# Kernel optimization log

Measured on AMD Instinct MI355X. Metric: run time of the kernel, lower is better.

## Reference

```python
import jax, jax.numpy as jnp
import numpy as np
from jax import lax

# 19 edges over 19 body-joint heatmap channels (0..18); PAF channels are 19..56
EDGES = np.array([[1,8],[8,9],[9,10],[1,11],[11,12],[12,13],[1,2],[2,3],[3,4],[2,16],
                  [1,5],[5,6],[6,7],[5,17],[0,1],[0,14],[0,15],[14,16],[15,17]], dtype=np.int32)
_i = np.arange(19, dtype=np.int32)
# per-edge 4 input channels: [node_a, node_b, paf_x(=19+2i), paf_y(=20+2i)]
CH_IDX = np.concatenate([EDGES, (19 + 2*_i)[:, None], (20 + 2*_i)[:, None]], axis=1)  # [19,4]

_W_SHAPES = [(16,4,5,5),(16,16,5,5),(32,16,5,5),(32,32,5,5),(32,32,5,5),(128,32,1,1),(2,128,1,1)]

def _conv(x, w, b):
    p = (w.shape[-1] - 1) // 2  # padding=2 for 5x5, 0 for 1x1
    y = lax.conv_general_dilated(x, w, window_strides=(1,1), padding=[(p,p),(p,p)],
                                 dimension_numbers=('NCHW','OIHW','NCHW'))
    return y + b[None, :, None, None]

def setup_inputs() -> dict:
    key = jax.random.key(0)
    keys = jax.random.split(key, 1 + 2*len(_W_SHAPES))
    N, C, H, W = 16, 57, 128, 128
    inp = {'cnn_output': jax.random.normal(keys[0], (N, C, H, W), dtype=jnp.float32),
           'gnn_interations': 1}
    for i, s in enumerate(_W_SHAPES):
        inp[f'w{i}'] = jax.random.normal(keys[1+2*i], s, dtype=jnp.float32) * 0.01
        inp[f'b{i}'] = jax.random.normal(keys[2+2*i], (s[0],), dtype=jnp.float32) * 0.01
    return inp

def reference(cnn_output, gnn_interations, w0, b0, w1, b1, w2, b2, w3, b3, w4, b4, w5, b5, w6, b6):
    N, _, H, Wd = cnn_output.shape
    ws = (w0, w1, w2, w3, w4, w5, w6)
    bs = (b0, b1, b2, b3, b4, b5, b6)
    # gather per-edge 4-channel inputs: [N,19,4,H,W] -> fold edges into batch
    x = cnn_output[:, jnp.asarray(CH_IDX)]            # [N,19,4,H,W]
    x = x.reshape(N * 19, 4, H, Wd)
    for i in range(7):
        x = _conv(x, ws[i], bs[i])
        if i != 6:
            x = jax.nn.relu(x)
    # edge n output (2 ch) -> output channels [2n, 2n+1]
    return x.reshape(N, 38, H, Wd)
```

## Files before the change

### kernel.cpp

```cpp
#include <hip/hip_runtime.h>
#include <hip/hip_bf16.h>

typedef __bf16  bf16x8 __attribute__((ext_vector_type(8)));
typedef float   f32x4  __attribute__((ext_vector_type(4)));
typedef int     i32x4  __attribute__((ext_vector_type(4)));
typedef int     i32x8  __attribute__((ext_vector_type(8)));

__device__ __constant__ int EDGE_A[19] = {1,8,9,1,11,12,1,2,3,2,1,5,6,5,0,0,0,14,15};
__device__ __constant__ int EDGE_B[19] = {8,9,10,11,12,13,2,3,4,16,5,6,7,17,1,14,15,16,17};

#define SACT  64.0f
#define SINV  (1.0f / 4096.0f)
#define SREQ  0.015625f
#define SCL1  0x7F7F7F7F

__device__ __forceinline__ unsigned short f2bf(float f) {
    unsigned int x = __float_as_uint(f);
    x += 0x7FFFu + ((x >> 16) & 1u);
    return (unsigned short)(x >> 16);
}
__device__ __forceinline__ unsigned int pack2(float a, float b) {
    __hip_bfloat162 t = __float22bfloat162_rn(make_float2(a, b));
    unsigned int r; __builtin_memcpy(&r, &t, 4); return r;
}
__device__ __forceinline__ unsigned char f2fp8(float v) {
    int r = __builtin_amdgcn_cvt_pk_fp8_f32(v, 0.f, 0, false);
    return (unsigned char)(r & 0xff);
}
__device__ __forceinline__ unsigned int pk4fp8(float a, float b, float c, float d) {
    int v = __builtin_amdgcn_cvt_pk_fp8_f32(a, b, 0, false);
    v = __builtin_amdgcn_cvt_pk_fp8_f32(c, d, v, true);
    return (unsigned int)v;
}
__device__ __forceinline__ unsigned int quant4(f32x4 a, float4 b, float s, bool oob) {
    float v0 = fmaxf(fmaf(a[0], s, b.x), 0.f);
    float v1 = fmaxf(fmaf(a[1], s, b.y), 0.f);
    float v2 = fmaxf(fmaf(a[2], s, b.z), 0.f);
    float v3 = fmaxf(fmaf(a[3], s, b.w), 0.f);
    unsigned int v = pk4fp8(v0, v1, v2, v3);
    return oob ? 0u : v;
}

__device__ __forceinline__ int sw8 (int l) { return l ^ ((l >> 4) & 8);  }
__device__ __forceinline__ int sw48(int l) { return l ^ ((l >> 3) & 48); }

__device__ __forceinline__ void store_relu4(unsigned char* dst, f32x4 a, float4 b, bool oob) {
    unsigned int lo = pack2(fmaxf(a[0] + b.x, 0.f), fmaxf(a[1] + b.y, 0.f));
    unsigned int hi = pack2(fmaxf(a[2] + b.z, 0.f), fmaxf(a[3] + b.w, 0.f));
    uint2 v; v.x = oob ? 0u : lo; v.y = oob ? 0u : hi;
    *(uint2*)dst = v;
}

extern "C" __global__ void __launch_bounds__(256)
reorder_weights(const float* __restrict__ w0, const float* __restrict__ w1,
                const float* __restrict__ w2, const float* __restrict__ w3,
                const float* __restrict__ w4, const float* __restrict__ w5,
                unsigned char* __restrict__ ws)
{
    int idx = blockIdx.x * 256 + threadIdx.x;
    unsigned short* wsS = (unsigned short*)ws;
    if (idx < 4096) {
        int k = idx & 31, oc = idx >> 5;
        wsS[idx] = f2bf(w5[oc * 32 + k]);
    } else if (idx < 6144) {
        int j = idx - 4096;
        int k = j & 31, n = (j >> 5) & 15, c = j >> 9;
        int t = c * 8 + (k >> 2), ic = k & 3;
        float v = (t < 25) ? w0[(n * 4 + ic) * 25 + t] : 0.f;
        wsS[idx] = f2bf(v);
    }
    if (idx < 6656) {
        int k = idx & 31, n = (idx >> 5) & 15, tp = idx >> 9;
        int t = 2 * tp + (k >> 4), ic = k & 15;
        float v = (t < 25) ? w1[(n * 16 + ic) * 25 + t] * SACT : 0.f;
        ws[12288 + idx] = f2fp8(v);
    } else if (idx < 19968) {
        int j = idx - 6656;
        int k = j & 31, n = (j >> 5) & 15, nt = (j >> 9) & 1, tp = j >> 10;
        int t = 2 * tp + (k >> 4), ic = k & 15, oc = nt * 16 + n;
        float v = (t < 25) ? w2[(oc * 16 + ic) * 25 + t] * SACT : 0.f;
        ws[18944 + j] = f2fp8(v);
    } else if (idx < 48640) {
        int j = idx - 19968;
        int tg = j >> 12, r = j & 4095;
        int nt = r >> 11, n = (r >> 7) & 15, q = (r >> 5) & 3, ic = r & 31;
        int tap = 4 * tg + q;
        float v = (tap < 25) ? w3[((nt * 16 + n) * 32 + ic) * 25 + tap] * SACT : 0.f;
        ws[32256 + j] = f2fp8(v);
    } else if (idx < 77312) {
        int j = idx - 48640;
        int tg = j >> 12, r = j & 4095;
        int nt = r >> 11, n = (r >> 7) & 15, q = (r >> 5) & 3, ic = r & 31;
        int tap = 4 * tg + q;
        float v = (tap < 25) ? w4[((nt * 16 + n) * 32 + ic) * 25 + tap] * SACT : 0.f;
        ws[60928 + j] = f2fp8(v);
    }
}

__device__ __forceinline__ void conv0_slab(
    const unsigned short* __restrict__ s_in, unsigned char* __restrict__ s0,
    const unsigned char* __restrict__ wB, const float* __restrict__ b0,
    int yoff, int oy, int ox, int wave, int lane)
{
    const int nl = lane & 15, quad = lane >> 4;
    const unsigned short* w0p = (const unsigned short*)(wB + 8192);
    bf16x8 wf[4];
#pragma unroll
    for (int c = 0; c < 4; ++c)
        wf[c] = *(const bf16x8*)(w0p + c * 512 + nl * 32 + quad * 8);
    float4 bb = *(const float4*)(b0 + quad * 4);
    float4 bbs = make_float4(bb.x * SACT, bb.y * SACT, bb.z * SACT, bb.w * SACT);

    int coff0[4], coff1[4];
#pragma unroll
    for (int c = 0; c < 4; ++c) {
        int t0 = c * 8 + quad * 2, t1 = t0 + 1;
        if (t0 > 24) t0 = 24;
        if (t1 > 24) t1 = 24;
        coff0[c] = ((t0 / 5) * 36 + (t0 % 5)) * 8;
        coff1[c] = ((t1 / 5) * 36 + (t1 % 5)) * 8;
    }
    const unsigned char* sB = (const unsigned char*)s_in;

#pragma unroll 1
    for (int i = 0; i < 9; ++i) {
        int mt = wave + 4 * i;
        int p = mt * 16 + nl;
        int y = p >> 5, x = p & 31;
        int abase = (y * 36 + x) * 8;
        f32x4 acc = (f32x4)0.f;
#pragma unroll
        for (int c = 0; c < 4; ++c) {
            uint2 lo = *(const uint2*)(sB + abase + coff0[c]);
            uint2 hi = *(const uint2*)(sB + abase + coff1[c]);
            bf16x8 a;
            ((uint2*)&a)[0] = lo; ((uint2*)&a)[1] = hi;
            acc = __builtin_amdgcn_mfma_f32_16x16x32_bf16(wf[c], a, acc, 0, 0, 0);
        }
        bool oob = ((unsigned)(oy - 8 + y + yoff) >= 128u) || ((unsigned)(ox - 8 + x) >= 128u);
        *(unsigned int*)(s0 + sw8(p * 16 + quad * 4)) = quant4(acc, bbs, SACT, oob);
    }
}

__device__ __forceinline__ void conv1_fp8(
    const unsigned char* __restrict__ s0, unsigned char* __restrict__ s1,
    const unsigned char* __restrict__ wB, const float* __restrict__ b1,
    int POFF, int gy0, int gx0, int wave, int lane)
{
    const int nl = lane & 15, quad = lane >> 4;
    const int h = quad >> 1, g8 = (quad & 1) * 8;

    int abase[7];
#pragma unroll
    for (int i = 0; i < 7; ++i) {
        int p = (wave + 4 * i) * 16 + nl;
        if (p > 391) p = 391;
        int y = p / 28, x = p - y * 28;
        abase[i] = (y * 32 + x) * 16 + g8;
    }
    f32x4 acc[7];
#pragma unroll
    for (int i = 0; i < 7; ++i) acc[i] = (f32x4)0.f;

    const unsigned char* wp = wB + 12288 + nl * 32 + quad * 8;

#pragma unroll 1
    for (int c0 = 0; c0 < 13; c0 += 5) {
        long wl[5];
#pragma unroll
        for (int tp = 0; tp < 5; ++tp)
            if (c0 + tp < 13) wl[tp] = *(const long*)(wp + (c0 + tp) * 512);
#pragma unroll
        for (int tp = 0; tp < 5; ++tp) {
            if (c0 + tp < 13) {
                int t = 2 * (c0 + tp) + h;
                if (t > 24) t = 24;
                int dy = t / 5, dx = t - 5 * dy;
                int toff = (dy * 32 + dx) * 16;
#pragma unroll
                for (int i = 0; i < 7; ++i)
                    if (wave + 4 * i < 25) {
                        long a = *(const long*)(s0 + sw8(abase[i] + toff));
                        acc[i] = __builtin_amdgcn_mfma_f32_16x16x32_fp8_fp8(wl[tp], a, acc[i], 0, 0, 0);
                    }
            }
        }
    }

    float4 bb = *(const float4*)(b1 + quad * 4);
    float4 bbs = make_float4(bb.x * SACT, bb.y * SACT, bb.z * SACT, bb.w * SACT);
#pragma unroll
    for (int i = 0; i < 7; ++i) {
        int p = (wave + 4 * i) * 16 + nl;
        if (p < 392) {
            int pg = p + POFF;
            int y = pg / 28, x = pg - y * 28;
            bool oob = ((unsigned)(gy0 + y) >= 128u) || ((unsigned)(gx0 + x) >= 128u);
            *(unsigned int*)(s1 + sw8(pg * 16 + quad * 4)) = quant4(acc[i], bbs, SREQ, oob);
        }
    }
}

template<int I0, int NI>
__device__ __forceinline__ void conv2_fp8(
    const unsigned char* __restrict__ s1, unsigned char* __restrict__ s2,
    const unsigned char* __restrict__ wA, const float* __restrict__ b2,
    int gy0, int gx0, int wave, int lane)
{
    const int nl = lane & 15, quad = lane >> 4;
    const int h = quad >> 1, g8 = (quad & 1) * 8;

    int abase[NI];
#pragma unroll
    for (int i = 0; i < NI; ++i) {
        int p = (wave + 4 * (I0 + i)) * 16 + nl;
        int y = p / 24, x = p - y * 24;
        abase[i] = (y * 28 + x) * 16 + g8;
    }
    f32x4 acc[NI][2];
#pragma unroll
    for (int i = 0; i < NI; ++i) { acc[i][0] = (f32x4)0.f; acc[i][1] = (f32x4)0.f; }

    const unsigned char* wp = wA + nl * 32 + quad * 8;

#pragma unroll 1
    for (int c0 = 0; c0 < 13; c0 += 3) {
        long wl[3][2];
#pragma unroll
        for (int tp = 0; tp < 3; ++tp)
            if (c0 + tp < 13) {
                wl[tp][0] = *(const long*)(wp + ((c0 + tp) * 2 + 0) * 512);
                wl[tp][1] = *(const long*)(wp + ((c0 + tp) * 2 + 1) * 512);
            }
#pragma unroll
        for (int tp = 0; tp < 3; ++tp) {
            if (c0 + tp < 13) {
                int t = 2 * (c0 + tp) + h;
                if (t > 24) t = 24;
                int dy = t / 5, dx = t - 5 * dy;
                int toff = (dy * 28 + dx) * 16;
#pragma unroll
                for (int i = 0; i < NI; ++i) {
                    long a = *(const long*)(s1 + sw8(abase[i] + toff));
                    acc[i][0] = __builtin_amdgcn_mfma_f32_16x16x32_fp8_fp8(wl[tp][0], a, acc[i][0], 0, 0, 0);
                    acc[i][1] = __builtin_amdgcn_mfma_f32_16x16x32_fp8_fp8(wl[tp][1], a, acc[i][1], 0, 0, 0);
                }
            }
        }
    }

#pragma unroll
    for (int i = 0; i < NI; ++i) {
        int p = (wave + 4 * (I0 + i)) * 16 + nl;
        int y = p / 24, x = p - y * 24;
        bool oob = ((unsigned)(gy0 + y) >= 128u) || ((unsigned)(gx0 + x) >= 128u);
#pragma unroll
        for (int nt = 0; nt < 2; ++nt) {
            float4 bb = *(const float4*)(b2 + nt * 16 + quad * 4);
            float4 bbs = make_float4(bb.x * SACT, bb.y * SACT, bb.z * SACT, bb.w * SACT);
            *(unsigned int*)(s2 + p * 48 + nt * 16 + quad * 4) =
                quant4(acc[i][nt], bbs, SREQ, oob);
        }
    }
}

template<int SINW, int SOUT, int MAXM, bool GUARD, bool FP8OUT>
__device__ __forceinline__ void conv_c32_mx(
    const unsigned char* __restrict__ sinB, unsigned char* __restrict__ soutB,
    const unsigned char* __restrict__ wA, const float* __restrict__ bias,
    int gy0, int gx0, int wave, int lane)
{
    constexpr int NM = (SOUT * SOUT) / 16;
    const int nl = lane & 15, quad = lane >> 4;

    int abase[MAXM];
#pragma unroll
    for (int i = 0; i < MAXM; ++i) {
        int p = (wave + 4 * i) * 16 + nl;
        if (GUARD && p > SOUT * SOUT - 1) p = SOUT * SOUT - 1;
        int y = p / SOUT, x = p - y * SOUT;
        abase[i] = (y * SINW + x) * 48;
    }
    f32x4 acc[MAXM][2];
#pragma unroll
    for (int i = 0; i < MAXM; ++i) { acc[i][0] = (f32x4)0.f; acc[i][1] = (f32x4)0.f; }

    const unsigned char* wp = wA + nl * 128 + quad * 32;

#pragma unroll 1
    for (int tg = 0; tg < 7; ++tg) {
        int t = 4 * tg + quad;
        if (t > 24) t = 24;
        int dy = t / 5, dx = t - 5 * dy;
        int to = (dy * SINW + dx) * 48;
        i32x8 wl0 = *(const i32x8*)(wp + tg * 4096);
        i32x8 wl1 = *(const i32x8*)(wp + tg * 4096 + 2048);
#pragma unroll
        for (int i = 0; i < MAXM; ++i)
            if (!GUARD || wave + 4 * i < NM) {
                i32x4 alo = *(const i32x4*)(sinB + abase[i] + to);
                i32x4 ahi = *(const i32x4*)(sinB + abase[i] + to + 16);
                i32x8 a;
                ((i32x4*)&a)[0] = alo; ((i32x4*)&a)[1] = ahi;
                acc[i][0] = __builtin_amdgcn_mfma_scale_f32_16x16x128_f8f6f4(
                                wl0, a, acc[i][0], 0, 0, 0, SCL1, 0, SCL1);
                acc[i][1] = __builtin_amdgcn_mfma_scale_f32_16x16x128_f8f6f4(
                                wl1, a, acc[i][1], 0, 0, 0, SCL1, 0, SCL1);
            }
    }

#pragma unroll
    for (int i = 0; i < MAXM; ++i) {
        int p = (wave + 4 * i) * 16 + nl;
        if (!GUARD || p < SOUT * SOUT) {
            int y = p / SOUT, x = p - y * SOUT;
            bool oob = ((unsigned)(gy0 + y) >= 128u) || ((unsigned)(gx0 + x) >= 128u);
#pragma unroll
            for (int nt = 0; nt < 2; ++nt) {
                float4 bb = *(const float4*)(bias + nt * 16 + quad * 4);
                if (FP8OUT) {
                    float4 bbs = make_float4(bb.x * SACT, bb.y * SACT, bb.z * SACT, bb.w * SACT);
                    *(unsigned int*)(soutB + p * 48 + nt * 16 + quad * 4) =
                        quant4(acc[i][nt], bbs, SREQ, oob);
                } else {
                    f32x4 s;
                    s[0] = acc[i][nt][0] * SINV; s[1] = acc[i][nt][1] * SINV;
                    s[2] = acc[i][nt][2] * SINV; s[3] = acc[i][nt][3] * SINV;
                    store_relu4(soutB + sw48(p * 64 + nt * 32 + quad * 8), s, bb, oob);
                }
            }
        }
    }
}

extern "C" __global__ void __launch_bounds__(256, 3)
gnn_paf_mfma(const float* __restrict__ cnn, const unsigned char* __restrict__ wB,
             const float* __restrict__ b0, const float* __restrict__ b1,
             const float* __restrict__ b2, const float* __restrict__ b3,
             const float* __restrict__ b4, const float* __restrict__ b5,
             const float* __restrict__ w6, const float* __restrict__ b6,
             float* __restrict__ out)
{
    __shared__ __align__(64) unsigned char smem[46848];
    unsigned char*  const s1   = smem;
    unsigned char*  const s3   = smem;
    unsigned short* const sin_ = (unsigned short*)(smem + 12544);
    unsigned char*  const s0   = smem + 19200;
    unsigned char*  const s2   = smem + 19200;
    unsigned char*  const s4   = smem + 19200;

    const int tid  = threadIdx.x;
    const int lane = tid & 63, wave = tid >> 6;
    const int tile = blockIdx.x, img = blockIdx.y;
    const int oy = (tile >> 3) * 16, ox = (tile & 7) * 16;
    const int n = img / 19, g = img - n * 19;
    const int ch0 = EDGE_A[g], ch1 = EDGE_B[g], ch2 = 19 + 2 * g, ch3 = 20 + 2 * g;
    const int nl = lane & 15, quad = lane >> 4;
    const long long nb = (long long)n * 57 * 16384;

    for (int idx = tid; idx < 792; idx += 256) {
        int r = idx / 36, c = idx - r * 36;
        int gy = oy - 10 + r, gx = ox - 10 + c;
        float v0 = 0.f, v1 = 0.f, v2 = 0.f, v3 = 0.f;
        if ((unsigned)gy < 128u && (unsigned)gx < 128u) {
            int off = gy * 128 + gx;
            v0 = cnn[nb + (long long)ch0 * 16384 + off];
            v1 = cnn[nb + (long long)ch1 * 16384 + off];
            v2 = cnn[nb + (long long)ch2 * 16384 + off];
            v3 = cnn[nb + (long long)ch3 * 16384 + off];
        }
        uint2 v; v.x = pack2(v0, v1); v.y = pack2(v2, v3);
        *(uint2*)(sin_ + idx * 4) = v;
    }
    __syncthreads();

    conv0_slab(sin_, s0, wB, b0, 0, oy, ox, wave, lane);
    __syncthreads();

    float gv[4][4];
#pragma unroll
    for (int j = 0; j < 4; ++j) {
        gv[j][0] = gv[j][1] = gv[j][2] = gv[j][3] = 0.f;
        int idx = tid + 256 * j;
        if (idx < 792) {
            int r = idx / 36, c = idx - r * 36;
            int gy = oy + 4 + r, gx = ox - 10 + c;
            if ((unsigned)gy < 128u && (unsigned)gx < 128u) {
                int off = gy * 128 + gx;
                gv[j][0] = cnn[nb + (long long)ch0 * 16384 + off];
                gv[j][1] = cnn[nb + (long long)ch1 * 16384 + off];
                gv[j][2] = cnn[nb + (long long)ch2 * 16384 + off];
                gv[j][3] = cnn[nb + (long long)ch3 * 16384 + off];
            }
        }
    }
    conv1_fp8(s0, s1, wB, b1, 0, oy - 6, ox - 6, wave, lane);
#pragma unroll
    for (int j = 0; j < 4; ++j) {
        int idx = tid + 256 * j;
        if (idx < 792) {
            uint2 v; v.x = pack2(gv[j][0], gv[j][1]); v.y = pack2(gv[j][2], gv[j][3]);
            *(uint2*)(sin_ + idx * 4) = v;
        }
    }
    __syncthreads();

    conv0_slab(sin_, s0, wB, b0, 14, oy, ox, wave, lane);
    __syncthreads();

    conv1_fp8(s0, s1, wB, b1, 392, oy - 6, ox - 6, wave, lane);
    __syncthreads();

    conv2_fp8<0, 5>(s1, s2, wB + 18944, b2, oy - 4, ox - 4, wave, lane);
    conv2_fp8<5, 4>(s1, s2, wB + 18944, b2, oy - 4, ox - 4, wave, lane);
    __syncthreads();

    conv_c32_mx<24, 20, 7, true,  true >(s2, s3, wB + 32256, b3, oy - 2, ox - 2, wave, lane);
    __syncthreads();

    conv_c32_mx<20, 16, 4, false, false>(s3, s4, wB + 60928, b4, oy, ox, wave, lane);
    __syncthreads();

    {
        const unsigned short* w5p = (const unsigned short*)wB;
        bf16x8 w5f[8];
#pragma unroll
        for (int nt = 0; nt < 8; ++nt)
            w5f[nt] = *(const bf16x8*)(w5p + nt * 512 + nl * 32 + quad * 8);
        const float b6q = b6[quad & 1];
#pragma unroll 1
        for (int ii = 0; ii < 4; ++ii) {
            int mt = wave + 4 * ii;
            int lin = (mt * 16 + nl) * 64 + quad * 16;
            bf16x8 pf = *(const bf16x8*)(s4 + sw48(lin));
            float o0 = 0.f, o1 = 0.f;
#pragma unroll
            for (int nt = 0; nt < 8; ++nt) {
                f32x4 acc = (f32x4)0.f;
                acc = __builtin_amdgcn_mfma_f32_16x16x32_bf16(w5f[nt], pf, acc, 0, 0, 0);
                float4 bb  = *(const float4*)(b5 + nt * 16 + quad * 4);
                float4 wa  = *(const float4*)(w6 + nt * 16 + quad * 4);
                float4 wb2 = *(const float4*)(w6 + 128 + nt * 16 + quad * 4);
                float h0 = fmaxf(acc[0] + bb.x, 0.f), h1 = fmaxf(acc[1] + bb.y, 0.f);
                float h2 = fmaxf(acc[2] + bb.z, 0.f), h3 = fmaxf(acc[3] + bb.w, 0.f);
                o0 = fmaf(h0, wa.x, fmaf(h1, wa.y, fmaf(h2, wa.z, fmaf(h3, wa.w, o0))));
                o1 = fmaf(h0, wb2.x, fmaf(h1, wb2.y, fmaf(h2, wb2.z, fmaf(h3, wb2.w, o1))));
            }
            o0 += __shfl_xor(o0, 16, 64); o0 += __shfl_xor(o0, 32, 64);
            o1 += __shfl_xor(o1, 16, 64); o1 += __shfl_xor(o1, 32, 64);
            if (quad < 2) {
                float val = ((quad == 0) ? o0 : o1) + b6q;
                long long ob = (((long long)n * 38 + 2 * g + quad) * 128 + (oy + mt)) * 128 + (ox + nl);
                out[ob] = val;
            }
        }
    }
}

extern "C" void kernel_launch(void* const* d_in, const int* in_sizes, int n_in,
                              void* d_out, int out_size, void* d_ws, size_t ws_size,
                              hipStream_t stream) {
    const float* cnn = (const float*)d_in[0];
    const float* w0 = (const float*)d_in[2];  const float* b0 = (const float*)d_in[3];
    const float* w1 = (const float*)d_in[4];  const float* b1 = (const float*)d_in[5];
    const float* w2 = (const float*)d_in[6];  const float* b2 = (const float*)d_in[7];
    const float* w3 = (const float*)d_in[8];  const float* b3 = (const float*)d_in[9];
    const float* w4 = (const float*)d_in[10]; const float* b4 = (const float*)d_in[11];
    const float* w5 = (const float*)d_in[12]; const float* b5 = (const float*)d_in[13];
    const float* w6 = (const float*)d_in[14]; const float* b6 = (const float*)d_in[15];
    float* out = (float*)d_out;
    unsigned char* wB = (unsigned char*)d_ws;

    hipLaunchKernelGGL(reorder_weights, dim3(302), dim3(256), 0, stream,
                       w0, w1, w2, w3, w4, w5, wB);
    hipLaunchKernelGGL(gnn_paf_mfma, dim3(64, 304), dim3(256), 0, stream,
                       cnn, wB, b0, b1, b2, b3, b4, b5, w6, b6, out);
}
```

Baseline: 1.170 ms.

## Switch conv1/conv2 to 16x16x128 scaled MFMA and shrink LDS for occupancy

Conv1 and conv2 move from 16x16x32 fp8 MFMA with two taps per instruction to the scaled 16x16x128 f8f6f4 MFMA covering eight taps per instruction, with the weight layouts reordered to match. The aim is to cut MFMA instruction count and LDS load count. The s2 buffer is packed to a 32-byte stride with an XOR swizzle, and the old sw8 swizzles are dropped. LDS drops from 46848 to 37632 bytes so launch bounds can request 4 blocks per CU instead of 3. The trade-offs are padded zero taps in the wider MFMAs, possible bank conflicts where swizzling was removed, and register pressure at the higher occupancy target.

New measurement: 1.390 ms. 1.19x slower.

```diff
diff --git a/kernel.cpp b/kernel.cpp
--- a/kernel.cpp
+++ b/kernel.cpp
@@ -41,7 +41,6 @@
     return oob ? 0u : v;
 }
 
-__device__ __forceinline__ int sw8 (int l) { return l ^ ((l >> 4) & 8);  }
 __device__ __forceinline__ int sw48(int l) { return l ^ ((l >> 3) & 48); }
 
 __device__ __forceinline__ void store_relu4(unsigned char* dst, f32x4 a, float4 b, bool oob) {
@@ -69,31 +68,31 @@
         float v = (t < 25) ? w0[(n * 4 + ic) * 25 + t] : 0.f;
         wsS[idx] = f2bf(v);
     }
-    if (idx < 6656) {
-        int k = idx & 31, n = (idx >> 5) & 15, tp = idx >> 9;
-        int t = 2 * tp + (k >> 4), ic = k & 15;
+    if (idx < 8192) {
+        int g = idx >> 11, n = (idx >> 7) & 15, q = (idx >> 5) & 3, b = idx & 31;
+        int t = 8 * g + 2 * q + (b >> 4), ic = b & 15;
         float v = (t < 25) ? w1[(n * 16 + ic) * 25 + t] * SACT : 0.f;
         ws[12288 + idx] = f2fp8(v);
-    } else if (idx < 19968) {
-        int j = idx - 6656;
-        int k = j & 31, n = (j >> 5) & 15, nt = (j >> 9) & 1, tp = j >> 10;
-        int t = 2 * tp + (k >> 4), ic = k & 15, oc = nt * 16 + n;
+    } else if (idx < 24576) {
+        int j = idx - 8192;
+        int g = j >> 12, nt = (j >> 11) & 1, n = (j >> 7) & 15, q = (j >> 5) & 3, b = j & 31;
+        int t = 8 * g + 2 * q + (b >> 4), ic = b & 15, oc = nt * 16 + n;
         float v = (t < 25) ? w2[(oc * 16 + ic) * 25 + t] * SACT : 0.f;
-        ws[18944 + j] = f2fp8(v);
-    } else if (idx < 48640) {
-        int j = idx - 19968;
+        ws[20480 + j] = f2fp8(v);
+    } else if (idx < 53248) {
+        int j = idx - 24576;
         int tg = j >> 12, r = j & 4095;
         int nt = r >> 11, n = (r >> 7) & 15, q = (r >> 5) & 3, ic = r & 31;
         int tap = 4 * tg + q;
         float v = (tap < 25) ? w3[((nt * 16 + n) * 32 + ic) * 25 + tap] * SACT : 0.f;
-        ws[32256 + j] = f2fp8(v);
-    } else if (idx < 77312) {
-        int j = idx - 48640;
+        ws[36864 + j] = f2fp8(v);
+    } else if (idx < 81920) {
+        int j = idx - 53248;
         int tg = j >> 12, r = j & 4095;
         int nt = r >> 11, n = (r >> 7) & 15, q = (r >> 5) & 3, ic = r & 31;
         int tap = 4 * tg + q;
         float v = (tap < 25) ? w4[((nt * 16 + n) * 32 + ic) * 25 + tap] * SACT : 0.f;
-        ws[60928 + j] = f2fp8(v);
+        ws[65536 + j] = f2fp8(v);
     }
 }
 
@@ -138,17 +137,16 @@
             acc = __builtin_amdgcn_mfma_f32_16x16x32_bf16(wf[c], a, acc, 0, 0, 0);
         }
         bool oob = ((unsigned)(oy - 8 + y + yoff) >= 128u) || ((unsigned)(ox - 8 + x) >= 128u);
-        *(unsigned int*)(s0 + sw8(p * 16 + quad * 4)) = quant4(acc, bbs, SACT, oob);
-    }
-}
-
-__device__ __forceinline__ void conv1_fp8(
+        *(unsigned int*)(s0 + p * 16 + quad * 4) = quant4(acc, bbs, SACT, oob);
+    }
+}
+
+__device__ __forceinline__ void conv1_mx(
     const unsigned char* __restrict__ s0, unsigned char* __restrict__ s1,
     const unsigned char* __restrict__ wB, const float* __restrict__ b1,
     int POFF, int gy0, int gx0, int wave, int lane)
 {
     const int nl = lane & 15, quad = lane >> 4;
-    const int h = quad >> 1, g8 = (quad & 1) * 8;
 
     int abase[7];
 #pragma unroll
@@ -156,35 +154,34 @@
         int p = (wave + 4 * i) * 16 + nl;
         if (p > 391) p = 391;
         int y = p / 28, x = p - y * 28;
-        abase[i] = (y * 32 + x) * 16 + g8;
+        abase[i] = (y * 32 + x) * 16;
     }
     f32x4 acc[7];
 #pragma unroll
     for (int i = 0; i < 7; ++i) acc[i] = (f32x4)0.f;
 
-    const unsigned char* wp = wB + 12288 + nl * 32 + quad * 8;
+    const unsigned char* wp = wB + 12288 + nl * 128 + quad * 32;
 
 #pragma unroll 1
-    for (int c0 = 0; c0 < 13; c0 += 5) {
-        long wl[5];
-#pragma unroll
-        for (int tp = 0; tp < 5; ++tp)
-            if (c0 + tp < 13) wl[tp] = *(const long*)(wp + (c0 + tp) * 512);
-#pragma unroll
-        for (int tp = 0; tp < 5; ++tp) {
-            if (c0 + tp < 13) {
-                int t = 2 * (c0 + tp) + h;
-                if (t > 24) t = 24;
-                int dy = t / 5, dx = t - 5 * dy;
-                int toff = (dy * 32 + dx) * 16;
-#pragma unroll
-                for (int i = 0; i < 7; ++i)
-                    if (wave + 4 * i < 25) {
-                        long a = *(const long*)(s0 + sw8(abase[i] + toff));
-                        acc[i] = __builtin_amdgcn_mfma_f32_16x16x32_fp8_fp8(wl[tp], a, acc[i], 0, 0, 0);
-                    }
-            }
-        }
+    for (int g = 0; g < 4; ++g) {
+        int t0 = 8 * g + 2 * quad, t1 = t0 + 1;
+        if (t0 > 24) t0 = 24;
+        if (t1 > 24) t1 = 24;
+        int dy0 = t0 / 5, dx0 = t0 - 5 * dy0;
+        int dy1 = t1 / 5, dx1 = t1 - 5 * dy1;
+        int to0 = (dy0 * 32 + dx0) * 16;
+        int to1 = (dy1 * 32 + dx1) * 16;
+        i32x8 wl = *(const i32x8*)(wp + g * 2048);
+#pragma unroll
+        for (int i = 0; i < 7; ++i)
+            if (wave + 4 * i < 25) {
+                i32x4 alo = *(const i32x4*)(s0 + abase[i] + to0);
+                i32x4 ahi = *(const i32x4*)(s0 + abase[i] + to1);
+                i32x8 a;
+                ((i32x4*)&a)[0] = alo; ((i32x4*)&a)[1] = ahi;
+                acc[i] = __builtin_amdgcn_mfma_scale_f32_16x16x128_f8f6f4(
+                             wl, a, acc[i], 0, 0, 0, SCL1, 0, SCL1);
+            }
     }
 
     float4 bb = *(const float4*)(b1 + quad * 4);
@@ -196,56 +193,53 @@
             int pg = p + POFF;
             int y = pg / 28, x = pg - y * 28;
             bool oob = ((unsigned)(gy0 + y) >= 128u) || ((unsigned)(gx0 + x) >= 128u);
-            *(unsigned int*)(s1 + sw8(pg * 16 + quad * 4)) = quant4(acc[i], bbs, SREQ, oob);
+            *(unsigned int*)(s1 + pg * 16 + quad * 4) = quant4(acc[i], bbs, SREQ, oob);
         }
     }
 }
 
 template<int I0, int NI>
-__device__ __forceinline__ void conv2_fp8(
+__device__ __forceinline__ void conv2_mx(
     const unsigned char* __restrict__ s1, unsigned char* __restrict__ s2,
-    const unsigned char* __restrict__ wA, const float* __restrict__ b2,
+    const unsigned char* __restrict__ wB, const float* __restrict__ b2,
     int gy0, int gx0, int wave, int lane)
 {
     const int nl = lane & 15, quad = lane >> 4;
-    const int h = quad >> 1, g8 = (quad & 1) * 8;
 
     int abase[NI];
 #pragma unroll
     for (int i = 0; i < NI; ++i) {
         int p = (wave + 4 * (I0 + i)) * 16 + nl;
         int y = p / 24, x = p - y * 24;
-        abase[i] = (y * 28 + x) * 16 + g8;
+        abase[i] = (y * 28 + x) * 16;
     }
     f32x4 acc[NI][2];
 #pragma unroll
     for (int i = 0; i < NI; ++i) { acc[i][0] = (f32x4)0.f; acc[i][1] = (f32x4)0.f; }
 
-    const unsigned char* wp = wA + nl * 32 + quad * 8;
+    const unsigned char* wp = wB + 20480 + nl * 128 + quad * 32;
 
 #pragma unroll 1
-    for (int c0 = 0; c0 < 13; c0 += 3) {
-        long wl[3][2];
-#pragma unroll
-        for (int tp = 0; tp < 3; ++tp)
-            if (c0 + tp < 13) {
-                wl[tp][0] = *(const long*)(wp + ((c0 + tp) * 2 + 0) * 512);
-                wl[tp][1] = *(const long*)(wp + ((c0 + tp) * 2 + 1) * 512);
-            }
-#pragma unroll
-        for (int tp = 0; tp < 3; ++tp) {
-            if (c0 + tp < 13) {
-                int t = 2 * (c0 + tp) + h;
-                if (t > 24) t = 24;
-                int dy = t / 5, dx = t - 5 * dy;
-                int toff = (dy * 28 + dx) * 16;
-#pragma unroll
-                for (int i = 0; i < NI; ++i) {
-                    long a = *(const long*)(s1 + sw8(abase[i] + toff));
-                    acc[i][0] = __builtin_amdgcn_mfma_f32_16x16x32_fp8_fp8(wl[tp][0], a, acc[i][0], 0, 0, 0);
-                    acc[i][1] = __builtin_amdgcn_mfma_f32_16x16x32_fp8_fp8(wl[tp][1], a, acc[i][1], 0, 0, 0);
-                }
-            }
+    for (int g = 0; g < 4; ++g) {
+        int t0 = 8 * g + 2 * quad, t1 = t0 + 1;
+        if (t0 > 24) t0 = 24;
+        if (t1 > 24) t1 = 24;
+        int dy0 = t0 / 5, dx0 = t0 - 5 * dy0;
+        int dy1 = t1 / 5, dx1 = t1 - 5 * dy1;
+        int to0 = (dy0 * 28 + dx0) * 16;
+        int to1 = (dy1 * 28 + dx1) * 16;
+        i32x8 wl0 = *(const i32x8*)(wp + g * 4096);
+        i32x8 wl1 = *(const i32x8*)(wp + g * 4096 + 2048);
+#pragma unroll
+        for (int i = 0; i < NI; ++i) {
+            i32x4 alo = *(const i32x4*)(s1 + abase[i] + to0);
+            i32x4 ahi = *(const i32x4*)(s1 + abase[i] + to1);
+            i32x8 a;
+            ((i32x4*)&a)[0] = alo; ((i32x4*)&a)[1] = ahi;
+            acc[i][0] = __builtin_amdgcn_mfma_scale_f32_16x16x128_f8f6f4(
+                            wl0, a, acc[i][0], 0, 0, 0, SCL1, 0, SCL1);
+            acc[i][1] = __builtin_amdgcn_mfma_scale_f32_16x16x128_f8f6f4(
+                            wl1, a, acc[i][1], 0, 0, 0, SCL1, 0, SCL1);
         }
     }
 
@@ -258,13 +252,13 @@
         for (int nt = 0; nt < 2; ++nt) {
             float4 bb = *(const float4*)(b2 + nt * 16 + quad * 4);
             float4 bbs = make_float4(bb.x * SACT, bb.y * SACT, bb.z * SACT, bb.w * SACT);
-            *(unsigned int*)(s2 + p * 48 + nt * 16 + quad * 4) =
-                quant4(acc[i][nt], bbs, SREQ, oob);
-        }
-    }
-}
-
-template<int SINW, int SOUT, int MAXM, bool GUARD, bool FP8OUT>
+            int byte = (p * 32 + nt * 16 + quad * 4) ^ ((p & 4) << 2);
+            *(unsigned int*)(s2 + byte) = quant4(acc[i][nt], bbs, SREQ, oob);
+        }
+    }
+}
+
+template<int SINW, int SOUT, int MAXM, bool GUARD, bool FP8OUT, bool INXOR, int INSTRIDE>
 __device__ __forceinline__ void conv_c32_mx(
     const unsigned char* __restrict__ sinB, unsigned char* __restrict__ soutB,
     const unsigned char* __restrict__ wA, const float* __restrict__ bias,
@@ -279,7 +273,7 @@
         int p = (wave + 4 * i) * 16 + nl;
         if (GUARD && p > SOUT * SOUT - 1) p = SOUT * SOUT - 1;
         int y = p / SOUT, x = p - y * SOUT;
-        abase[i] = (y * SINW + x) * 48;
+        abase[i] = (y * SINW + x) * INSTRIDE;
     }
     f32x4 acc[MAXM][2];
 #pragma unroll
@@ -292,14 +286,16 @@
         int t = 4 * tg + quad;
         if (t > 24) t = 24;
         int dy = t / 5, dx = t - 5 * dy;
-        int to = (dy * SINW + dx) * 48;
+        int to = (dy * SINW + dx) * INSTRIDE;
         i32x8 wl0 = *(const i32x8*)(wp + tg * 4096);
         i32x8 wl1 = *(const i32x8*)(wp + tg * 4096 + 2048);
 #pragma unroll
         for (int i = 0; i < MAXM; ++i)
             if (!GUARD || wave + 4 * i < NM) {
-                i32x4 alo = *(const i32x4*)(sinB + abase[i] + to);
-                i32x4 ahi = *(const i32x4*)(sinB + abase[i] + to + 16);
+                int ad = abase[i] + to;
+                if (INXOR) ad ^= (ad >> 3) & 16;
+                i32x4 alo = *(const i32x4*)(sinB + ad);
+                i32x4 ahi = *(const i32x4*)(sinB + (INXOR ? (ad ^ 16) : (ad + 16)));
                 i32x8 a;
                 ((i32x4*)&a)[0] = alo; ((i32x4*)&a)[1] = ahi;
                 acc[i][0] = __builtin_amdgcn_mfma_scale_f32_16x16x128_f8f6f4(
@@ -333,7 +329,7 @@
     }
 }
 
-extern "C" __global__ void __launch_bounds__(256, 3)
+extern "C" __global__ void __launch_bounds__(256, 4)
 gnn_paf_mfma(const float* __restrict__ cnn, const unsigned char* __restrict__ wB,
              const float* __restrict__ b0, const float* __restrict__ b1,
              const float* __restrict__ b2, const float* __restrict__ b3,
@@ -341,12 +337,12 @@
              const float* __restrict__ w6, const float* __restrict__ b6,
              float* __restrict__ out)
 {
-    __shared__ __align__(64) unsigned char smem[46848];
+    __shared__ __align__(64) unsigned char smem[37632];
     unsigned char*  const s1   = smem;
+    unsigned short* const sin_ = (unsigned short*)(smem + 12544);
+    unsigned char*  const s0   = smem + 18880;
+    unsigned char*  const s2   = smem + 19200;
     unsigned char*  const s3   = smem;
-    unsigned short* const sin_ = (unsigned short*)(smem + 12544);
-    unsigned char*  const s0   = smem + 19200;
-    unsigned char*  const s2   = smem + 19200;
     unsigned char*  const s4   = smem + 19200;
 
     const int tid  = threadIdx.x;
@@ -394,7 +390,7 @@
             }
         }
     }
-    conv1_fp8(s0, s1, wB, b1, 0, oy - 6, ox - 6, wave, lane);
+    conv1_mx(s0, s1, wB, b1, 0, oy - 6, ox - 6, wave, lane);
 #pragma unroll
     for (int j = 0; j < 4; ++j) {
         int idx = tid + 256 * j;
@@ -408,17 +404,17 @@
     conv0_slab(sin_, s0, wB, b0, 14, oy, ox, wave, lane);
     __syncthreads();
 
-    conv1_fp8(s0, s1, wB, b1, 392, oy - 6, ox - 6, wave, lane);
-    __syncthreads();
-
-    conv2_fp8<0, 5>(s1, s2, wB + 18944, b2, oy - 4, ox - 4, wave, lane);
-    conv2_fp8<5, 4>(s1, s2, wB + 18944, b2, oy - 4, ox - 4, wave, lane);
-    __syncthreads();
-
-    conv_c32_mx<24, 20, 7, true,  true >(s2, s3, wB + 32256, b3, oy - 2, ox - 2, wave, lane);
-    __syncthreads();
-
-    conv_c32_mx<20, 16, 4, false, false>(s3, s4, wB + 60928, b4, oy, ox, wave, lane);
+    conv1_mx(s0, s1, wB, b1, 392, oy - 6, ox - 6, wave, lane);
+    __syncthreads();
+
+    conv2_mx<0, 5>(s1, s2, wB, b2, oy - 4, ox - 4, wave, lane);
+    conv2_mx<5, 4>(s1, s2, wB, b2, oy - 4, ox - 4, wave, lane);
+    __syncthreads();
+
+    conv_c32_mx<24, 20, 7, true,  true,  true,  32>(s2, s3, wB + 36864, b3, oy - 2, ox - 2, wave, lane);
+    __syncthreads();
+
+    conv_c32_mx<20, 16, 4, false, false, false, 48>(s3, s4, wB + 65536, b4, oy, ox, wave, lane);
     __syncthreads();
 
     {
@@ -471,7 +467,7 @@
     float* out = (float*)d_out;
     unsigned char* wB = (unsigned char*)d_ws;
 
-    hipLaunchKernelGGL(reorder_weights, dim3(302), dim3(256), 0, stream,
+    hipLaunchKernelGGL(reorder_weights, dim3(320), dim3(256), 0, stream,
                        w0, w1, w2, w3, w4, w5, wB);
     hipLaunchKernelGGL(gnn_paf_mfma, dim3(64, 304), dim3(256), 0, stream,
                        cnn, wB, b0, b1, b2, b3, b4, b5, w6, b6, out);
```
